# Kernel tuning notes

Measured on AMD Instinct MI355X. Metric: run time of the kernel, lower is better.

## Reference

```python
import jax, jax.numpy as jnp
import numpy as np
from jax.ops import segment_sum, segment_max

N_NODES = 50000
N_EDGES = 800000
B = 1024            # number of graphs
NODE_DIM = 21
ESM_DIM = 480
TAB_DIM = 7
H = 128             # hidden_dim
LSTM_H = H // 2     # 64 per direction
NEG_SLOPE = 0.2
BN_EPS = 1e-5


def setup_inputs() -> dict:
    key = jax.random.key(0)
    ks = iter(jax.random.split(key, 48))
    r = lambda shape, s=0.05: (s * jax.random.normal(next(ks), shape)).astype(jnp.float32)
    inp = {
        'x': jax.random.normal(next(ks), (N_NODES, NODE_DIM), dtype=jnp.float32),
        'edge_index': jax.random.randint(next(ks), (2, N_EDGES), 0, N_NODES, dtype=jnp.int64),
        'batch': jnp.sort(jax.random.randint(next(ks), (N_NODES,), 0, B, dtype=jnp.int64)),
        'esm_emb': jax.random.normal(next(ks), (B, ESM_DIM), dtype=jnp.float32),
        'tab_feats': jax.random.normal(next(ks), (B, TAB_DIM), dtype=jnp.float32),
        # GATConv 1 (heads=1)
        'gat1_W': r((H, NODE_DIM)), 'gat1_asrc': r((H,)), 'gat1_adst': r((H,)), 'gat1_b': r((H,)),
        # GATConv 2
        'gat2_W': r((H, H)), 'gat2_asrc': r((H,)), 'gat2_adst': r((H,)), 'gat2_b': r((H,)),
        # Bidirectional LSTM (seq_len=1, so a single cell step per direction)
        'lstm_Wih_f': r((4 * LSTM_H, ESM_DIM)), 'lstm_Whh_f': r((4 * LSTM_H, LSTM_H)),
        'lstm_bih_f': r((4 * LSTM_H,)), 'lstm_bhh_f': r((4 * LSTM_H,)),
        'lstm_Wih_r': r((4 * LSTM_H, ESM_DIM)), 'lstm_Whh_r': r((4 * LSTM_H, LSTM_H)),
        'lstm_bih_r': r((4 * LSTM_H,)), 'lstm_bhh_r': r((4 * LSTM_H,)),
        # tabular net
        'tab_W': r((64, TAB_DIM)), 'tab_b': r((64,)), 'tab_bn_g': jnp.ones((64,), jnp.float32), 'tab_bn_b': jnp.zeros((64,), jnp.float32),
        # fusion head
        'fus1_W': r((256, 320)), 'fus1_b': r((256,)), 'fus_bn_g': jnp.ones((256,), jnp.float32), 'fus_bn_b': jnp.zeros((256,), jnp.float32),
        'fus2_W': r((128, 256)), 'fus2_b': r((128,)),
        'fus3_W': r((1, 128)), 'fus3_b': r((1,)),
    }
    return inp


def _gat(h_in, src, dst, W, a_src, a_dst, bias):
    # PyG GATConv, heads=1, concat=True, self-loops already appended.
    h = h_in @ W.T                                  # [N, H]
    alpha_s = h @ a_src                             # [N]
    alpha_d = h @ a_dst                             # [N]
    e = jax.nn.leaky_relu(alpha_s[src] + alpha_d[dst], NEG_SLOPE)  # [E]
    m = segment_max(e, dst, num_segments=N_NODES)   # stable softmax per target
    ex = jnp.exp(e - m[dst])
    den = segment_sum(ex, dst, num_segments=N_NODES)
    coef = ex / (den[dst] + 1e-16)
    out = segment_sum(coef[:, None] * h[src], dst, num_segments=N_NODES)
    return out + bias


def _bn(x, g, b):
    # BatchNorm1d in training mode: biased batch statistics
    mu = jnp.mean(x, axis=0)
    var = jnp.var(x, axis=0)
    return (x - mu) * jax.lax.rsqrt(var + BN_EPS) * g + b


def _lstm_step(x, Wih, Whh, bih, bhh):
    # single step with zero initial (h, c); Whh term vanishes but kept for fidelity
    g = x @ Wih.T + bih + jnp.zeros((x.shape[0], Whh.shape[1]), x.dtype) @ Whh.T + bhh
    i, f, gg, o = jnp.split(g, 4, axis=1)           # PyTorch gate order i,f,g,o
    c = jax.nn.sigmoid(i) * jnp.tanh(gg)
    return jax.nn.sigmoid(o) * jnp.tanh(c)


def reference(x, edge_index, batch, esm_emb, tab_feats,
              gat1_W, gat1_asrc, gat1_adst, gat1_b,
              gat2_W, gat2_asrc, gat2_adst, gat2_b,
              lstm_Wih_f, lstm_Whh_f, lstm_bih_f, lstm_bhh_f,
              lstm_Wih_r, lstm_Whh_r, lstm_bih_r, lstm_bhh_r,
              tab_W, tab_b, tab_bn_g, tab_bn_b,
              fus1_W, fus1_b, fus_bn_g, fus_bn_b,
              fus2_W, fus2_b, fus3_W, fus3_b):
    sl = jnp.arange(N_NODES, dtype=edge_index.dtype)
    src = jnp.concatenate([edge_index[0], sl])      # add_self_loops=True default
    dst = jnp.concatenate([edge_index[1], sl])

    h1 = jax.nn.relu(_gat(x, src, dst, gat1_W, gat1_asrc, gat1_adst, gat1_b))
    h2 = jax.nn.relu(_gat(h1, src, dst, gat2_W, gat2_asrc, gat2_adst, gat2_b))

    counts = segment_sum(jnp.ones((N_NODES,), h2.dtype), batch, num_segments=B)
    graph_embed = segment_sum(h2, batch, num_segments=B) / jnp.maximum(counts, 1.0)[:, None]

    # bilstm over seq_len=1: output at last (only) step = concat(fwd, bwd)
    h_f = _lstm_step(esm_emb, lstm_Wih_f, lstm_Whh_f, lstm_bih_f, lstm_bhh_f)
    h_r = _lstm_step(esm_emb, lstm_Wih_r, lstm_Whh_r, lstm_bih_r, lstm_bhh_r)
    seq_embed = jnp.concatenate([h_f, h_r], axis=1)  # [B, 128]

    tab_embed = jax.nn.relu(_bn(tab_feats @ tab_W.T + tab_b, tab_bn_g, tab_bn_b))

    z = jnp.concatenate([graph_embed, seq_embed, tab_embed], axis=1)  # [B, 320]
    z = jax.nn.relu(_bn(z @ fus1_W.T + fus1_b, fus_bn_g, fus_bn_b))   # dropout: identity (eval)
    z = jax.nn.relu(z @ fus2_W.T + fus2_b)
    return z @ fus3_W.T + fus3_b                     # [B, 1]
```

## Files before the change

### kernel.cpp

```cpp
#include <hip/hip_runtime.h>
#include <hip/hip_bf16.h>

#define N_NODES 50000
#define N_PAD   50048
#define N_EDGES 800000
#define E_TOT   850000
#define NB      1024
#define ESM_DIM 480
#define HD      128
#define NBUCK   196
#define CAP     5120
#define EPB     3321
#define SC_BLK  256
#define CVT_BLK 256
#define BND_BLK 196
#define WC_BLK  16
#define TAB_BLK 4
#define G1B     782
#define LSTM_B  96
#define LG      384
#define AGG_GRID 12500
#define NL_BLK  512

typedef short short8 __attribute__((ext_vector_type(8)));
typedef unsigned short ushort8 __attribute__((ext_vector_type(8)));
typedef float f32x4 __attribute__((ext_vector_type(4)));

__device__ __forceinline__ float bf2f(unsigned int u) {
    union { unsigned int i; float f; } c; c.i = u << 16; return c.f;
}
__device__ __forceinline__ unsigned short f2bf(float f) {
    union { float f; unsigned int i; } c; c.f = f;
    unsigned int i = c.i;
    return (unsigned short)((i + 0x7FFFu + ((i >> 16) & 1u)) >> 16);
}
__device__ __forceinline__ void split2(float v, unsigned short& h, unsigned short& l) {
    h = f2bf(v);
    l = f2bf(v - bf2f(h));
}


__device__ void dev_scatter(const int* __restrict__ ei, int* __restrict__ gcur,
                            int* __restrict__ pairs, int blk) {
    __shared__ int hist[NBUCK];
    int t = threadIdx.x;
    for (int u = t; u < NBUCK; u += 256) hist[u] = 0;
    __syncthreads();
    int e0 = blk * EPB;
    int e1 = (e0 + EPB < E_TOT) ? e0 + EPB : E_TOT;
    for (int e = e0 + t; e < e1; e += 256) {
        int d = (e < N_EDGES) ? ei[N_EDGES + e] : (e - N_EDGES);
        atomicAdd(&hist[d >> 8], 1);
    }
    __syncthreads();
    for (int u = t; u < NBUCK; u += 256) {
        int c = hist[u];
        hist[u] = (c > 0) ? atomicAdd(&gcur[u], c) : 0;
    }
    __syncthreads();
    for (int e = e0 + t; e < e1; e += 256) {
        int s, d;
        if (e < N_EDGES) { s = ei[e]; d = ei[N_EDGES + e]; }
        else             { s = d = e - N_EDGES; }
        int bu = d >> 8;
        int pos = atomicAdd(&hist[bu], 1);
        pairs[bu * CAP + pos] = s | ((d & 255) << 16);
    }
}

__device__ void dev_cvt(const float* __restrict__ esm,
                        const float* __restrict__ Wf,
                        const float* __restrict__ Wr,
                        const float* __restrict__ W1,
                        unsigned short* __restrict__ esm_h, unsigned short* __restrict__ esm_l,
                        unsigned short* __restrict__ wg_h,  unsigned short* __restrict__ wg_l,
                        unsigned short* __restrict__ w1h,   unsigned short* __restrict__ w1l,
                        int blk) {
    int tid = blk * 256 + threadIdx.x;
    for (int u = tid; u < NB * 120; u += CVT_BLK * 256) {
        float4 v = ((const float4*)esm)[u];
        ushort4 h, l;
        split2(v.x, h.x, l.x); split2(v.y, h.y, l.y);
        split2(v.z, h.z, l.z); split2(v.w, h.w, l.w);
        ((ushort4*)esm_h)[u] = h; ((ushort4*)esm_l)[u] = l;
    }
    for (int u = tid; u < LG * 120; u += CVT_BLK * 256) {
        int n = u / 120, kk = u - n * 120;
        int rr = (n >= 192) ? n - 192 : n;
        const float* Ws = (n >= 192) ? Wr : Wf;
        int srow = (rr < 64) ? rr : rr + 64;
        float4 v = *(const float4*)&Ws[(size_t)srow * 480 + kk * 4];
        ushort4 h, l;
        split2(v.x, h.x, l.x); split2(v.y, h.y, l.y);
        split2(v.z, h.z, l.z); split2(v.w, h.w, l.w);
        ((ushort4*)wg_h)[u] = h; ((ushort4*)wg_l)[u] = l;
    }
    for (int u = tid; u < 128 * 32; u += CVT_BLK * 256) {
        int f = u >> 5, k = u & 31;
        float v = (k < 21) ? W1[f * 21 + k] : 0.f;
        unsigned short h, l;
        split2(v, h, l);
        w1h[u] = h; w1l[u] = l;
    }
}

__device__ void dev_tab4(const float* __restrict__ tf, const float* __restrict__ W,
                         const float* __restrict__ bias, const float* __restrict__ g,
                         const float* __restrict__ b, float* __restrict__ z, int blk) {
    __shared__ float ssum[16][16];
    __shared__ float ssq[16][16];
    int t = threadIdx.x;
    int rg = t >> 4, jl = t & 15;
    int j = blk * 16 + jl;
    float Wj[7];
#pragma unroll
    for (int k = 0; k < 7; ++k) Wj[k] = W[j * 7 + k];
    float bj = bias[j];
    float s = 0.f, q = 0.f;
    for (int rr = 0; rr < 64; ++rr) {
        int row = rg * 64 + rr;
        const float* xp = &tf[(size_t)row * 7];
        float a = bj;
#pragma unroll
        for (int k = 0; k < 7; ++k) a += xp[k] * Wj[k];
        s += a; q += a * a;
    }
    ssum[rg][jl] = s; ssq[rg][jl] = q;
    __syncthreads();
    for (int off = 8; off; off >>= 1) {
        if (rg < off) { ssum[rg][jl] += ssum[rg + off][jl]; ssq[rg][jl] += ssq[rg + off][jl]; }
        __syncthreads();
    }
    float mu = ssum[0][jl] * (1.f / 1024.f);
    float var = ssq[0][jl] * (1.f / 1024.f) - mu * mu;
    float sc = rsqrtf(var + 1e-5f) * g[j];
    float sh = b[j] - mu * sc;
    for (int rr = 0; rr < 64; ++rr) {
        int row = rg * 64 + rr;
        const float* xp = &tf[(size_t)row * 7];
        float a = bj;
#pragma unroll
        for (int k = 0; k < 7; ++k) a += xp[k] * Wj[k];
        z[(size_t)row * 320 + 256 + j] = fmaxf(a * sc + sh, 0.f);
    }
}

__global__ __launch_bounds__(256) void megaA(
        const int* __restrict__ ei, int* __restrict__ gcur, int* __restrict__ pairs,
        const float* __restrict__ esm, const float* __restrict__ Wih_f,
        const float* __restrict__ Wih_r, const float* __restrict__ gat1_W,
        unsigned short* __restrict__ esm_h, unsigned short* __restrict__ esm_l,
        unsigned short* __restrict__ wg_h,  unsigned short* __restrict__ wg_l,
        unsigned short* __restrict__ w1h,   unsigned short* __restrict__ w1l,
        const int* __restrict__ batch, int* __restrict__ gstart,
        const float* __restrict__ W2, unsigned short* __restrict__ Wb,
        const float* __restrict__ tf, const float* __restrict__ tab_W,
        const float* __restrict__ tab_b, const float* __restrict__ tab_g,
        const float* __restrict__ tab_bb, float* __restrict__ z) {
    int b = blockIdx.x, t = threadIdx.x;
    if (b < SC_BLK) {
        dev_scatter(ei, gcur, pairs, b);
    } else if (b < SC_BLK + CVT_BLK) {
        dev_cvt(esm, Wih_f, Wih_r, gat1_W, esm_h, esm_l, wg_h, wg_l, w1h, w1l, b - SC_BLK);
    } else if (b < SC_BLK + CVT_BLK + BND_BLK) {
        int i = (b - (SC_BLK + CVT_BLK)) * 256 + t;
        if (i >= N_NODES) return;
        int bb = batch[i];
        int bp = (i == 0) ? -1 : batch[i - 1];
        for (int g = bp + 1; g <= bb; ++g) gstart[g] = i;
        if (i == N_NODES - 1)
            for (int g = bb + 1; g <= NB; ++g) gstart[g] = N_NODES;
    } else if (b < SC_BLK + CVT_BLK + BND_BLK + WC_BLK) {
        int i = (b - (SC_BLK + CVT_BLK + BND_BLK)) * 256 + t;
        if (i >= 128 * 32) return;
        float4 v = ((const float4*)W2)[i];
        ((ushort4*)Wb)[i] = make_ushort4(f2bf(v.x), f2bf(v.y), f2bf(v.z), f2bf(v.w));
    } else {
        dev_tab4(tf, tab_W, tab_b, tab_g, tab_bb, z,
                 b - (SC_BLK + CVT_BLK + BND_BLK + WC_BLK));
    }
}


__device__ __forceinline__ float sigmoidf_(float x) { return 1.f / (1.f + __expf(-x)); }

__device__ void dev_gat1_mfma(const float* __restrict__ X,
                              const unsigned short* __restrict__ w1h,
                              const unsigned short* __restrict__ w1l,
                              const float* __restrict__ asrc, const float* __restrict__ adst,
                              unsigned short* __restrict__ out,
                              float* __restrict__ alpha_s, float* __restrict__ alpha_d,
                              int blk) {
    int t = threadIdx.x;
    int wid = t >> 6, L = t & 63, quad = L >> 4, lo = L & 15;
    int m0 = blk * 64 + wid * 16;
    int row = m0 + lo;
    const float* xr = X + (size_t)row * 21;
    int kbase = quad * 8;
    bool valid = row < N_NODES;
    float xv[8];
#pragma unroll
    for (int j = 0; j < 8; ++j) {
        int k = kbase + j;
        xv[j] = (valid && k < 21) ? xr[k] : 0.f;
    }
    short8 ah, al;
#pragma unroll
    for (int j = 0; j < 8; ++j) {
        unsigned short h, l;
        split2(xv[j], h, l);
        ah[j] = (short)h; al[j] = (short)l;
    }
    float as_p[4] = {0.f, 0.f, 0.f, 0.f};
    float ad_p[4] = {0.f, 0.f, 0.f, 0.f};
#pragma unroll
    for (int ft = 0; ft < 8; ++ft) {
        short8 bh = *(const short8*)&w1h[(ft * 16 + lo) * 32 + kbase];
        short8 bl = *(const short8*)&w1l[(ft * 16 + lo) * 32 + kbase];
        f32x4 acc = {0.f, 0.f, 0.f, 0.f};
        acc = __builtin_amdgcn_mfma_f32_16x16x32_bf16(ah, bh, acc, 0, 0, 0);
        acc = __builtin_amdgcn_mfma_f32_16x16x32_bf16(al, bh, acc, 0, 0, 0);
        acc = __builtin_amdgcn_mfma_f32_16x16x32_bf16(ah, bl, acc, 0, 0, 0);
        float asv = asrc[ft * 16 + lo];
        float adv = adst[ft * 16 + lo];
#pragma unroll
        for (int r = 0; r < 4; ++r) {
            int m = m0 + quad * 4 + r;
            out[(size_t)m * HD + ft * 16 + lo] = f2bf(acc[r]);
            as_p[r] += acc[r] * asv;
            ad_p[r] += acc[r] * adv;
        }
    }
#pragma unroll
    for (int off = 1; off < 16; off <<= 1) {
#pragma unroll
        for (int r = 0; r < 4; ++r) {
            as_p[r] += __shfl_xor(as_p[r], off);
            ad_p[r] += __shfl_xor(ad_p[r], off);
        }
    }
    if (lo == 0) {
#pragma unroll
        for (int r = 0; r < 4; ++r) {
            int m = m0 + quad * 4 + r;
            if (m < N_NODES) { alpha_s[m] = as_p[r]; alpha_d[m] = ad_p[r]; }
        }
    }
}

__device__ void dev_lstm_mfma(const unsigned short* __restrict__ Ah,
                              const unsigned short* __restrict__ Al,
                              const unsigned short* __restrict__ Bh,
                              const unsigned short* __restrict__ Bl,
                              float* __restrict__ G, int blk) {
    __shared__ unsigned short Bsh[64][104];
    __shared__ unsigned short Bsl[64][104];
    int t = threadIdx.x;
    int wid = t >> 6, L = t & 63, quad = L >> 4, lo = L & 15;
    int nt = blk % 6, mt = blk / 6;
    int m0 = mt * 64 + wid * 16;
    int n0 = nt * 64;
    f32x4 accs[4];
#pragma unroll
    for (int ft = 0; ft < 4; ++ft) accs[ft] = (f32x4){0.f, 0.f, 0.f, 0.f};
    const unsigned short* arh = Ah + (size_t)(m0 + lo) * ESM_DIM;
    const unsigned short* arl = Al + (size_t)(m0 + lo) * ESM_DIM;
    for (int c = 0; c < 5; ++c) {
        int k0c = c * 96;
        short8 ah[3], al[3];
#pragma unroll
        for (int ks = 0; ks < 3; ++ks) {
            ah[ks] = *(const short8*)&arh[k0c + ks * 32 + quad * 8];
            al[ks] = *(const short8*)&arl[k0c + ks * 32 + quad * 8];
        }
#pragma unroll
        for (int u = 0; u < 3; ++u) {
            int li = u * 2048 + t * 8;
            int row = li / 96, col = li % 96;
            *(ushort8*)&Bsh[row][col] =
                *(const ushort8*)&Bh[(size_t)(n0 + row) * ESM_DIM + k0c + col];
            *(ushort8*)&Bsl[row][col] =
                *(const ushort8*)&Bl[(size_t)(n0 + row) * ESM_DIM + k0c + col];
        }
        __syncthreads();
#pragma unroll
        for (int ks = 0; ks < 3; ++ks) {
#pragma unroll
            for (int ft = 0; ft < 4; ++ft) {
                short8 bh = *(const short8*)&Bsh[ft * 16 + lo][ks * 32 + quad * 8];
                short8 bl = *(const short8*)&Bsl[ft * 16 + lo][ks * 32 + quad * 8];
                accs[ft] = __builtin_amdgcn_mfma_f32_16x16x32_bf16(ah[ks], bh, accs[ft], 0, 0, 0);
                accs[ft] = __builtin_amdgcn_mfma_f32_16x16x32_bf16(al[ks], bh, accs[ft], 0, 0, 0);
                accs[ft] = __builtin_amdgcn_mfma_f32_16x16x32_bf16(ah[ks], bl, accs[ft], 0, 0, 0);
            }
        }
        __syncthreads();
    }
#pragma unroll
    for (int ft = 0; ft < 4; ++ft) {
#pragma unroll
        for (int r = 0; r < 4; ++r)
            G[(size_t)(m0 + quad * 4 + r) * LG + n0 + ft * 16 + lo] = accs[ft][r];
    }
}

__global__ __launch_bounds__(256) void megaB(
        const int* __restrict__ gcur, const int* __restrict__ pairs,
        int* __restrict__ row_beg, int* __restrict__ row_end, int* __restrict__ csr_src,
        const float* __restrict__ x,
        const unsigned short* __restrict__ w1h, const unsigned short* __restrict__ w1l,
        const float* __restrict__ gat1_as, const float* __restrict__ gat1_ad,
        unsigned short* __restrict__ h0, float* __restrict__ alpha_s, float* __restrict__ alpha_d,
        const unsigned short* __restrict__ esm_h, const unsigned short* __restrict__ esm_l,
        const unsigned short* __restrict__ wg_h,  const unsigned short* __restrict__ wg_l,
        float* __restrict__ g_lstm) {
    int b = blockIdx.x, t = threadIdx.x;
    if (b < NBUCK) {
        __shared__ int dc[256];
        __shared__ int wt[4];
        __shared__ int cur[256];
        int rs = b * CAP;
        int re = rs + gcur[b];
        dc[t] = 0;
        __syncthreads();
        for (int i = rs + t; i < re; i += 1024) {
            int i1 = i + 256, i2 = i + 512, i3 = i + 768;
            int p0 = pairs[i];
            int p1 = (i1 < re) ? pairs[i1] : 0;
            int p2 = (i2 < re) ? pairs[i2] : 0;
            int p3 = (i3 < re) ? pairs[i3] : 0;
            atomicAdd(&dc[p0 >> 16], 1);
            if (i1 < re) atomicAdd(&dc[p1 >> 16], 1);
            if (i2 < re) atomicAdd(&dc[p2 >> 16], 1);
            if (i3 < re) atomicAdd(&dc[p3 >> 16], 1);
        }
        __syncthreads();
        int v = dc[t];
        int lane = t & 63, wid = t >> 6;
        int sc = v;
#pragma unroll
        for (int off = 1; off < 64; off <<= 1) {
            int n = __shfl_up(sc, off);
            if (lane >= off) sc += n;
        }
        if (lane == 63) wt[wid] = sc;
        __syncthreads();
        int pref = 0;
        for (int ww = 0; ww < wid; ++ww) pref += wt[ww];
        int beg = rs + pref + sc - v;
        int node = b * 256 + t;
        if (node < N_NODES) { row_beg[node] = beg; row_end[node] = beg + v; }
        cur[t] = beg;
        __syncthreads();
        for (int i = rs + t; i < re; i += 1024) {
            int i1 = i + 256, i2 = i + 512, i3 = i + 768;
            int p0 = pairs[i];
            int p1 = (i1 < re) ? pairs[i1] : 0;
            int p2 = (i2 < re) ? pairs[i2] : 0;
            int p3 = (i3 < re) ? pairs[i3] : 0;
            int pos0 = atomicAdd(&cur[p0 >> 16], 1);
            csr_src[pos0] = p0 & 0xFFFF;
            if (i1 < re) { int pos = atomicAdd(&cur[p1 >> 16], 1); csr_src[pos] = p1 & 0xFFFF; }
            if (i2 < re) { int pos = atomicAdd(&cur[p2 >> 16], 1); csr_src[pos] = p2 & 0xFFFF; }
            if (i3 < re) { int pos = atomicAdd(&cur[p3 >> 16], 1); csr_src[pos] = p3 & 0xFFFF; }
        }
    } else if (b < NBUCK + LSTM_B) {
        dev_lstm_mfma(esm_h, esm_l, wg_h, wg_l, g_lstm, b - NBUCK);
    } else {
        dev_gat1_mfma(x, w1h, w1l, gat1_as, gat1_ad, h0, alpha_s, alpha_d,
                      b - (NBUCK + LSTM_B));
    }
}


__global__ __launch_bounds__(256) void gemm_mfma(const unsigned short* __restrict__ A,
                                                 const unsigned short* __restrict__ Wb,
                                                 const float* __restrict__ asrc,
                                                 const float* __restrict__ adst,
                                                 unsigned short* __restrict__ out,
                                                 float* __restrict__ alpha_s,
                                                 float* __restrict__ alpha_d, int M) {
    __shared__ unsigned short Wlds[128 * 136];
    int t = threadIdx.x;
    for (int u = t; u < 128 * 16; u += 256) {
        int row = u >> 4, seg = u & 15;
        *(ushort8*)&Wlds[row * 136 + seg * 8] = *(const ushort8*)&Wb[row * 128 + seg * 8];
    }
    __syncthreads();
    int wid = t >> 6, L = t & 63;
    int quad = L >> 4, lo = L & 15;
    int m0 = blockIdx.x * 64 + wid * 16;
    short8 afrag[4];
#pragma unroll
    for (int ch = 0; ch < 4; ++ch)
        afrag[ch] = *(const short8*)&A[(size_t)(m0 + lo) * HD + ch * 32 + quad * 8];
    float as_p[4] = {0.f, 0.f, 0.f, 0.f};
    float ad_p[4] = {0.f, 0.f, 0.f, 0.f};
#pragma unroll
    for (int ft = 0; ft < 8; ++ft) {
        f32x4 acc = {0.f, 0.f, 0.f, 0.f};
#pragma unroll
        for (int ch = 0; ch < 4; ++ch) {
            short8 b = *(const short8*)&Wlds[(ft * 16 + lo) * 136 + ch * 32 + quad * 8];
            acc = __builtin_amdgcn_mfma_f32_16x16x32_bf16(afrag[ch], b, acc, 0, 0, 0);
        }
        float asv = asrc[ft * 16 + lo];
        float adv = adst[ft * 16 + lo];
#pragma unroll
        for (int r = 0; r < 4; ++r) {
            int m = m0 + quad * 4 + r;
            if (m < M) out[(size_t)m * HD + ft * 16 + lo] = f2bf(acc[r]);
            as_p[r] += acc[r] * asv;
            ad_p[r] += acc[r] * adv;
        }
    }
#pragma unroll
    for (int off = 1; off < 16; off <<= 1) {
#pragma unroll
        for (int r = 0; r < 4; ++r) {
            as_p[r] += __shfl_xor(as_p[r], off);
            ad_p[r] += __shfl_xor(ad_p[r], off);
        }
    }
    if (lo == 0) {
#pragma unroll
        for (int r = 0; r < 4; ++r) {
            int m = m0 + quad * 4 + r;
            if (m < M) { alpha_s[m] = as_p[r]; alpha_d[m] = ad_p[r]; }
        }
    }
}


__global__ void gat_spmm(const unsigned short* __restrict__ h, const int* __restrict__ row_beg,
                         const int* __restrict__ row_end, const int* __restrict__ csr_src,
                         const float* __restrict__ alpha_s, const float* __restrict__ alpha_d,
                         const float* __restrict__ bias, unsigned short* __restrict__ outp,
                         const float* __restrict__ g_lstm,
                         const float* __restrict__ bihf, const float* __restrict__ bhhf,
                         const float* __restrict__ bihr, const float* __restrict__ bhhr,
                         float* __restrict__ z) {
    if (blockIdx.x >= AGG_GRID) {
        int idx = (blockIdx.x - AGG_GRID) * 256 + threadIdx.x;
        int bb = idx >> 7, jj = idx & 127;
        int dir = jj >> 6, j = jj & 63;
        const float* gb = g_lstm + (size_t)bb * LG + dir * 192;
        const float* bi = dir ? bihr : bihf;
        const float* bh = dir ? bhhr : bhhf;
        float gi = gb[j]        + bi[j]        + bh[j];
        float gg = gb[64 + j]   + bi[128 + j]  + bh[128 + j];
        float go = gb[128 + j]  + bi[192 + j]  + bh[192 + j];
        float c = sigmoidf_(gi) * tanhf(gg);
        z[(size_t)bb * 320 + 128 + jj] = sigmoidf_(go) * tanhf(c);
        return;
    }
    int w = (int)((blockIdx.x * (size_t)blockDim.x + threadIdx.x) >> 6);
    int lane = threadIdx.x & 63;
    if (w >= N_NODES) return;
    int grp = lane >> 4, l16 = lane & 15;
    int rs = row_beg[w], re = row_end[w];
    int deg = re - rs;
    float ad = alpha_d[w];
    float acc[8] = {0.f, 0.f, 0.f, 0.f, 0.f, 0.f, 0.f, 0.f};
    if (deg <= 64) {
        int s_reg = 0;
        float e = -1e30f;
        if (lane < deg) {
            s_reg = csr_src[rs + lane];
            float t0 = alpha_s[s_reg] + ad;
            e = (t0 > 0.f) ? t0 : 0.2f * t0;
        }
        float m = e;
#pragma unroll
        for (int off = 32; off; off >>= 1) m = fmaxf(m, __shfl_xor(m, off));
        float ex = (lane < deg) ? __expf(e - m) : 0.f;
        float den = ex;
#pragma unroll
        for (int off = 32; off; off >>= 1) den += __shfl_xor(den, off);
        float coef = ex / (den + 1e-16f);
        int i = rs + grp;
        for (; i + 4 < re; i += 8) {
            int idx = i - rs;
            float c0 = __shfl(coef, idx);
            int   s0 = __shfl(s_reg, idx);
            float c1 = __shfl(coef, idx + 4);
            int   s1 = __shfl(s_reg, idx + 4);
            ushort8 h0 = *(const ushort8*)&h[(size_t)s0 * HD + l16 * 8];
            ushort8 h1 = *(const ushort8*)&h[(size_t)s1 * HD + l16 * 8];
#pragma unroll
            for (int j = 0; j < 8; ++j) acc[j] += c0 * bf2f(h0[j]);
#pragma unroll
            for (int j = 0; j < 8; ++j) acc[j] += c1 * bf2f(h1[j]);
        }
        if (i < re) {
            int idx = i - rs;
            float c0 = __shfl(coef, idx);
            int   s0 = __shfl(s_reg, idx);
            ushort8 h0 = *(const ushort8*)&h[(size_t)s0 * HD + l16 * 8];
#pragma unroll
            for (int j = 0; j < 8; ++j) acc[j] += c0 * bf2f(h0[j]);
        }
    } else {
        float m = -1e30f;
        for (int i = rs + lane; i < re; i += 64) {
            int s = csr_src[i];
            float t0 = alpha_s[s] + ad;
            t0 = (t0 > 0.f) ? t0 : 0.2f * t0;
            m = fmaxf(m, t0);
        }
#pragma unroll
        for (int off = 32; off; off >>= 1) m = fmaxf(m, __shfl_xor(m, off));
        float den = 0.f;
        for (int i = rs + lane; i < re; i += 64) {
            int s = csr_src[i];
            float t0 = alpha_s[s] + ad;
            t0 = (t0 > 0.f) ? t0 : 0.2f * t0;
            den += __expf(t0 - m);
        }
#pragma unroll
        for (int off = 32; off; off >>= 1) den += __shfl_xor(den, off);
        float inv = 1.f / (den + 1e-16f);
        for (int i = rs + grp; i < re; i += 4) {
            int s = csr_src[i];
            float t0 = alpha_s[s] + ad;
            t0 = (t0 > 0.f) ? t0 : 0.2f * t0;
            float c = __expf(t0 - m) * inv;
            ushort8 hv = *(const ushort8*)&h[(size_t)s * HD + l16 * 8];
#pragma unroll
            for (int j = 0; j < 8; ++j) acc[j] += c * bf2f(hv[j]);
        }
    }
#pragma unroll
    for (int j = 0; j < 8; ++j) {
        acc[j] += __shfl_xor(acc[j], 16);
        acc[j] += __shfl_xor(acc[j], 32);
    }
    int f0 = l16 * 8 + grp * 2;
    float2 bv = *(const float2*)&bias[f0];
    float vx = fmaxf(acc[grp * 2]     + bv.x, 0.f);
    float vy = fmaxf(acc[grp * 2 + 1] + bv.y, 0.f);
    unsigned int pv = (unsigned int)f2bf(vx) | ((unsigned int)f2bf(vy) << 16);
    *(unsigned int*)&outp[(size_t)w * HD + f0] = pv;
}


__global__ void pool_kernel(const unsigned short* __restrict__ h, const int* __restrict__ start,
                            float* __restrict__ z) {
    int w = (int)((blockIdx.x * (size_t)blockDim.x + threadIdx.x) >> 6);
    int lane = threadIdx.x & 63;
    if (w >= NB) return;
    int grp = lane >> 4, l16 = lane & 15;
    int s0 = start[w], s1 = start[w + 1];
    float acc[8] = {0.f, 0.f, 0.f, 0.f, 0.f, 0.f, 0.f, 0.f};
    int n = s0 + grp;
    for (; n + 4 < s1; n += 8) {
        ushort8 a = *(const ushort8*)&h[(size_t)n * HD + l16 * 8];
        ushort8 b = *(const ushort8*)&h[(size_t)(n + 4) * HD + l16 * 8];
#pragma unroll
        for (int j = 0; j < 8; ++j) acc[j] += bf2f(a[j]);
#pragma unroll
        for (int j = 0; j < 8; ++j) acc[j] += bf2f(b[j]);
    }
    if (n < s1) {
        ushort8 a = *(const ushort8*)&h[(size_t)n * HD + l16 * 8];
#pragma unroll
        for (int j = 0; j < 8; ++j) acc[j] += bf2f(a[j]);
    }
#pragma unroll
    for (int j = 0; j < 8; ++j) {
        acc[j] += __shfl_xor(acc[j], 16);
        acc[j] += __shfl_xor(acc[j], 32);
    }
    float inv = 1.f / fmaxf((float)(s1 - s0), 1.f);
    int f0 = l16 * 8 + grp * 2;
    *(float2*)&z[(size_t)w * 320 + f0] =
        make_float2(acc[grp * 2] * inv, acc[grp * 2 + 1] * inv);
}
// ... 92 lines not shown
            *(float4*)&Ws[wf][wk] = *(const float4*)&W2[(size_t)wf * 256 + kc + wk];
        }
        __syncthreads();
#pragma unroll
        for (int k = 0; k < 32; ++k) {
            float w = Ws[f][k];
#pragma unroll
            for (int r = 0; r < 8; ++r) acc[r] += Xs[rh * 8 + r][k] * w;
        }
        __syncthreads();
    }
    float bv = b2[f], wv = W3[f];
    if (t < 16) rowsum[t] = 0.f;
    __syncthreads();
#pragma unroll
    for (int r = 0; r < 8; ++r) {
        float v = fmaxf(acc[r] + bv, 0.f) * wv;
#pragma unroll
        for (int off = 32; off; off >>= 1) v += __shfl_xor(v, off);
        if ((t & 63) == 0) atomicAdd(&rowsum[rh * 8 + r], v);
    }
    __syncthreads();
    if (t < 16) out[r0 + t] = rowsum[t] + b3[0];
}


extern "C" void kernel_launch(void* const* d_in, const int* in_sizes, int n_in,
                              void* d_out, int out_size, void* d_ws, size_t ws_size,
                              hipStream_t stream) {
    const float* x        = (const float*)d_in[0];
    const int*   ei       = (const int*)d_in[1];
    const int*   batch    = (const int*)d_in[2];
    const float* esm      = (const float*)d_in[3];
    const float* tabf     = (const float*)d_in[4];
    const float* gat1_W   = (const float*)d_in[5];
    const float* gat1_as  = (const float*)d_in[6];
    const float* gat1_ad  = (const float*)d_in[7];
    const float* gat1_b   = (const float*)d_in[8];
    const float* gat2_W   = (const float*)d_in[9];
    const float* gat2_as  = (const float*)d_in[10];
    const float* gat2_ad  = (const float*)d_in[11];
    const float* gat2_b   = (const float*)d_in[12];
    const float* Wih_f    = (const float*)d_in[13];
    const float* bih_f    = (const float*)d_in[15];
    const float* bhh_f    = (const float*)d_in[16];
    const float* Wih_r    = (const float*)d_in[17];
    const float* bih_r    = (const float*)d_in[19];
    const float* bhh_r    = (const float*)d_in[20];
    const float* tab_W    = (const float*)d_in[21];
    const float* tab_b    = (const float*)d_in[22];
    const float* tab_g    = (const float*)d_in[23];
    const float* tab_bb   = (const float*)d_in[24];
    const float* fus1_W   = (const float*)d_in[25];
    const float* fus_g    = (const float*)d_in[27];
    const float* fus_bb   = (const float*)d_in[28];
    const float* fus2_W   = (const float*)d_in[29];
    const float* fus2_b   = (const float*)d_in[30];
    const float* fus3_W   = (const float*)d_in[31];
    const float* fus3_b   = (const float*)d_in[32];
    float* out = (float*)d_out;

    char* ws = (char*)d_ws;
    size_t off = 0;
    auto alloc = [&](size_t bytes) -> char* {
        char* p = ws + off;
        off += (bytes + 255) & ~(size_t)255;
        return p;
    };
    unsigned short* h0_bf = (unsigned short*)alloc((size_t)N_PAD * HD * 2);
    unsigned short* hA_bf = (unsigned short*)alloc((size_t)N_PAD * HD * 2);
    unsigned short* h2_bf = (unsigned short*)alloc((size_t)N_PAD * HD * 2);
    unsigned short* h_act = (unsigned short*)alloc((size_t)N_NODES * HD * 2);
    float* alpha_s = (float*)alloc((size_t)N_NODES * 4);
    float* alpha_d = (float*)alloc((size_t)N_NODES * 4);
    unsigned short* w2bf = (unsigned short*)alloc((size_t)HD * HD * 2);
    int*   row_beg = (int*)alloc((size_t)N_NODES * 4);
    int*   row_end = (int*)alloc((size_t)N_NODES * 4);
    int*   csr_src = (int*)alloc((size_t)NBUCK * CAP * 4);
    int*   pairs   = (int*)alloc((size_t)NBUCK * CAP * 4);
    int*   gstart  = (int*)alloc((size_t)(NB + 1) * 4);
    float* z1pre   = (float*)alloc((size_t)NB * 256 * 4);
    float* z       = (float*)alloc((size_t)NB * 320 * 4);
    float* g_lstm  = (float*)alloc((size_t)NB * LG * 4);
    unsigned short* esm_h = (unsigned short*)alloc((size_t)NB * ESM_DIM * 2);
    unsigned short* esm_l = (unsigned short*)alloc((size_t)NB * ESM_DIM * 2);
    unsigned short* wg_h  = (unsigned short*)alloc((size_t)LG * ESM_DIM * 2);
    unsigned short* wg_l  = (unsigned short*)alloc((size_t)LG * ESM_DIM * 2);
    unsigned short* w1h   = (unsigned short*)alloc((size_t)128 * 32 * 2);
    unsigned short* w1l   = (unsigned short*)alloc((size_t)128 * 32 * 2);
    int*   gcur    = (int*)alloc((size_t)NBUCK * 4);
    float* colsum  = (float*)alloc((size_t)256 * 4);
    float* colsq   = (float*)alloc((size_t)256 * 4);
    size_t zero_len = (size_t)((char*)colsq + 256 * 4 - (char*)gcur);
    hipMemsetAsync(gcur, 0, zero_len, stream);

    megaA<<<SC_BLK + CVT_BLK + BND_BLK + WC_BLK + TAB_BLK, 256, 0, stream>>>(
        ei, gcur, pairs, esm, Wih_f, Wih_r, gat1_W,
        esm_h, esm_l, wg_h, wg_l, w1h, w1l,
        batch, gstart, gat2_W, w2bf,
        tabf, tab_W, tab_b, tab_g, tab_bb, z);

    megaB<<<NBUCK + LSTM_B + G1B, 256, 0, stream>>>(
        gcur, pairs, row_beg, row_end, csr_src,
        x, w1h, w1l, gat1_as, gat1_ad, h0_bf, alpha_s, alpha_d,
        esm_h, esm_l, wg_h, wg_l, g_lstm);

    gat_spmm<<<AGG_GRID + NL_BLK, 256, 0, stream>>>(h0_bf, row_beg, row_end, csr_src,
                                                    alpha_s, alpha_d, gat1_b, hA_bf,
                                                    g_lstm, bih_f, bhh_f, bih_r, bhh_r, z);

    gemm_mfma<<<N_PAD / 64, 256, 0, stream>>>(hA_bf, w2bf, gat2_as, gat2_ad,
                                              h2_bf, alpha_s, alpha_d, N_NODES);

    gat_spmm<<<AGG_GRID, 256, 0, stream>>>(h2_bf, row_beg, row_end, csr_src,
                                           alpha_s, alpha_d, gat2_b, h_act,
                                           g_lstm, bih_f, bhh_f, bih_r, bhh_r, z);

    pool_kernel<<<(NB + 3) / 4, 256, 0, stream>>>(h_act, gstart, z);

    fus1_stats<<<dim3(64, 4), 256, 0, stream>>>(z, fus1_W, z1pre, colsum, colsq);

    fus2_final<<<64, 256, 0, stream>>>(z1pre, colsum, colsq, fus_g, fus_bb,
                                       fus2_W, fus2_b, fus3_W, fus3_b, out);

    (void)in_sizes; (void)n_in; (void)out_size; (void)ws_size;
}
```

Measured before the change: 292.3 us.

## Fuse bf16 split conversion into GAT1/LSTM consumers and move them into first launch

Removes the separate conversion pass that pre-split esm embeddings and weights into bf16 hi/lo buffers. The GAT1 and LSTM MFMA kernels now read fp32 and split in-register, and both move into the first mega-launch, so the second launch only builds the CSR. The edge scatter caches each thread's packed edges in registers to avoid re-reading edge_index, and the SpMM inner loop is unrolled to four neighbours. The cost is redundant conversion work per block and higher register pressure in the scatter and SpMM.

```diff
diff --git a/kernel.cpp b/kernel.cpp
--- a/kernel.cpp
+++ b/kernel.cpp
@@ -12,7 +12,6 @@
 #define CAP     5120
 #define EPB     3321
 #define SC_BLK  256
-#define CVT_BLK 256
 #define BND_BLK 196
 #define WC_BLK  16
 #define TAB_BLK 4
@@ -48,9 +47,18 @@
     __syncthreads();
     int e0 = blk * EPB;
     int e1 = (e0 + EPB < E_TOT) ? e0 + EPB : E_TOT;
-    for (int e = e0 + t; e < e1; e += 256) {
-        int d = (e < N_EDGES) ? ei[N_EDGES + e] : (e - N_EDGES);
-        atomicAdd(&hist[d >> 8], 1);
+    int ec[13];
+#pragma unroll
+    for (int u = 0; u < 13; ++u) {
+        int e = e0 + t + u * 256;
+        if (e < e1) {
+            int s, d;
+            if (e < N_EDGES) { s = ei[e]; d = ei[N_EDGES + e]; }
+            else             { s = d = e - N_EDGES; }
+            int bu = d >> 8;
+            ec[u] = s | ((d & 255) << 16) | (bu << 24);
+            atomicAdd(&hist[bu], 1);
+        }
     }
     __syncthreads();
     for (int u = t; u < NBUCK; u += 256) {
@@ -58,135 +66,20 @@
         hist[u] = (c > 0) ? atomicAdd(&gcur[u], c) : 0;
     }
     __syncthreads();
-    for (int e = e0 + t; e < e1; e += 256) {
-        int s, d;
-        if (e < N_EDGES) { s = ei[e]; d = ei[N_EDGES + e]; }
-        else             { s = d = e - N_EDGES; }
-        int bu = d >> 8;
-        int pos = atomicAdd(&hist[bu], 1);
-        pairs[bu * CAP + pos] = s | ((d & 255) << 16);
-    }
-}
-
-__device__ void dev_cvt(const float* __restrict__ esm,
-                        const float* __restrict__ Wf,
-                        const float* __restrict__ Wr,
-                        const float* __restrict__ W1,
-                        unsigned short* __restrict__ esm_h, unsigned short* __restrict__ esm_l,
-                        unsigned short* __restrict__ wg_h,  unsigned short* __restrict__ wg_l,
-                        unsigned short* __restrict__ w1h,   unsigned short* __restrict__ w1l,
-                        int blk) {
-    int tid = blk * 256 + threadIdx.x;
-    for (int u = tid; u < NB * 120; u += CVT_BLK * 256) {
-        float4 v = ((const float4*)esm)[u];
-        ushort4 h, l;
-        split2(v.x, h.x, l.x); split2(v.y, h.y, l.y);
-        split2(v.z, h.z, l.z); split2(v.w, h.w, l.w);
-        ((ushort4*)esm_h)[u] = h; ((ushort4*)esm_l)[u] = l;
-    }
-    for (int u = tid; u < LG * 120; u += CVT_BLK * 256) {
-        int n = u / 120, kk = u - n * 120;
-        int rr = (n >= 192) ? n - 192 : n;
-        const float* Ws = (n >= 192) ? Wr : Wf;
-        int srow = (rr < 64) ? rr : rr + 64;
-        float4 v = *(const float4*)&Ws[(size_t)srow * 480 + kk * 4];
-        ushort4 h, l;
-        split2(v.x, h.x, l.x); split2(v.y, h.y, l.y);
-        split2(v.z, h.z, l.z); split2(v.w, h.w, l.w);
-        ((ushort4*)wg_h)[u] = h; ((ushort4*)wg_l)[u] = l;
-    }
-    for (int u = tid; u < 128 * 32; u += CVT_BLK * 256) {
-        int f = u >> 5, k = u & 31;
-        float v = (k < 21) ? W1[f * 21 + k] : 0.f;
-        unsigned short h, l;
-        split2(v, h, l);
-        w1h[u] = h; w1l[u] = l;
-    }
-}
-
-__device__ void dev_tab4(const float* __restrict__ tf, const float* __restrict__ W,
-                         const float* __restrict__ bias, const float* __restrict__ g,
-                         const float* __restrict__ b, float* __restrict__ z, int blk) {
-    __shared__ float ssum[16][16];
-    __shared__ float ssq[16][16];
-    int t = threadIdx.x;
-    int rg = t >> 4, jl = t & 15;
-    int j = blk * 16 + jl;
-    float Wj[7];
-#pragma unroll
-    for (int k = 0; k < 7; ++k) Wj[k] = W[j * 7 + k];
-    float bj = bias[j];
-    float s = 0.f, q = 0.f;
-    for (int rr = 0; rr < 64; ++rr) {
-        int row = rg * 64 + rr;
-        const float* xp = &tf[(size_t)row * 7];
-        float a = bj;
-#pragma unroll
-        for (int k = 0; k < 7; ++k) a += xp[k] * Wj[k];
-        s += a; q += a * a;
-    }
-    ssum[rg][jl] = s; ssq[rg][jl] = q;
-    __syncthreads();
-    for (int off = 8; off; off >>= 1) {
-        if (rg < off) { ssum[rg][jl] += ssum[rg + off][jl]; ssq[rg][jl] += ssq[rg + off][jl]; }
-        __syncthreads();
-    }
-    float mu = ssum[0][jl] * (1.f / 1024.f);
-    float var = ssq[0][jl] * (1.f / 1024.f) - mu * mu;
-    float sc = rsqrtf(var + 1e-5f) * g[j];
-    float sh = b[j] - mu * sc;
-    for (int rr = 0; rr < 64; ++rr) {
-        int row = rg * 64 + rr;
-        const float* xp = &tf[(size_t)row * 7];
-        float a = bj;
-#pragma unroll
-        for (int k = 0; k < 7; ++k) a += xp[k] * Wj[k];
-        z[(size_t)row * 320 + 256 + j] = fmaxf(a * sc + sh, 0.f);
-    }
-}
-
-__global__ __launch_bounds__(256) void megaA(
-        const int* __restrict__ ei, int* __restrict__ gcur, int* __restrict__ pairs,
-        const float* __restrict__ esm, const float* __restrict__ Wih_f,
-        const float* __restrict__ Wih_r, const float* __restrict__ gat1_W,
-        unsigned short* __restrict__ esm_h, unsigned short* __restrict__ esm_l,
-        unsigned short* __restrict__ wg_h,  unsigned short* __restrict__ wg_l,
-        unsigned short* __restrict__ w1h,   unsigned short* __restrict__ w1l,
-        const int* __restrict__ batch, int* __restrict__ gstart,
-        const float* __restrict__ W2, unsigned short* __restrict__ Wb,
-        const float* __restrict__ tf, const float* __restrict__ tab_W,
-        const float* __restrict__ tab_b, const float* __restrict__ tab_g,
-        const float* __restrict__ tab_bb, float* __restrict__ z) {
-    int b = blockIdx.x, t = threadIdx.x;
-    if (b < SC_BLK) {
-        dev_scatter(ei, gcur, pairs, b);
-    } else if (b < SC_BLK + CVT_BLK) {
-        dev_cvt(esm, Wih_f, Wih_r, gat1_W, esm_h, esm_l, wg_h, wg_l, w1h, w1l, b - SC_BLK);
-    } else if (b < SC_BLK + CVT_BLK + BND_BLK) {
-        int i = (b - (SC_BLK + CVT_BLK)) * 256 + t;
-        if (i >= N_NODES) return;
-        int bb = batch[i];
-        int bp = (i == 0) ? -1 : batch[i - 1];
-        for (int g = bp + 1; g <= bb; ++g) gstart[g] = i;
-        if (i == N_NODES - 1)
-            for (int g = bb + 1; g <= NB; ++g) gstart[g] = N_NODES;
-    } else if (b < SC_BLK + CVT_BLK + BND_BLK + WC_BLK) {
-        int i = (b - (SC_BLK + CVT_BLK + BND_BLK)) * 256 + t;
-        if (i >= 128 * 32) return;
-        float4 v = ((const float4*)W2)[i];
-        ((ushort4*)Wb)[i] = make_ushort4(f2bf(v.x), f2bf(v.y), f2bf(v.z), f2bf(v.w));
-    } else {
-        dev_tab4(tf, tab_W, tab_b, tab_g, tab_bb, z,
-                 b - (SC_BLK + CVT_BLK + BND_BLK + WC_BLK));
-    }
-}
-
-
-__device__ __forceinline__ float sigmoidf_(float x) { return 1.f / (1.f + __expf(-x)); }
+#pragma unroll
+    for (int u = 0; u < 13; ++u) {
+        int e = e0 + t + u * 256;
+        if (e < e1) {
+            int val = ec[u];
+            int bu = ((unsigned)val) >> 24;
+            int pos = atomicAdd(&hist[bu], 1);
+            pairs[bu * CAP + pos] = val & 0xFFFFFF;
+        }
+    }
+}
 
 __device__ void dev_gat1_mfma(const float* __restrict__ X,
-                              const unsigned short* __restrict__ w1h,
-                              const unsigned short* __restrict__ w1l,
+                              const float* __restrict__ W1,
                               const float* __restrict__ asrc, const float* __restrict__ adst,
                               unsigned short* __restrict__ out,
                               float* __restrict__ alpha_s, float* __restrict__ alpha_d,
@@ -198,25 +91,29 @@
     const float* xr = X + (size_t)row * 21;
     int kbase = quad * 8;
     bool valid = row < N_NODES;
-    float xv[8];
+    short8 ah, al;
 #pragma unroll
     for (int j = 0; j < 8; ++j) {
         int k = kbase + j;
-        xv[j] = (valid && k < 21) ? xr[k] : 0.f;
-    }
-    short8 ah, al;
-#pragma unroll
-    for (int j = 0; j < 8; ++j) {
+        float v = (valid && k < 21) ? xr[k] : 0.f;
         unsigned short h, l;
-        split2(xv[j], h, l);
+        split2(v, h, l);
         ah[j] = (short)h; al[j] = (short)l;
     }
     float as_p[4] = {0.f, 0.f, 0.f, 0.f};
     float ad_p[4] = {0.f, 0.f, 0.f, 0.f};
 #pragma unroll
     for (int ft = 0; ft < 8; ++ft) {
-        short8 bh = *(const short8*)&w1h[(ft * 16 + lo) * 32 + kbase];
-        short8 bl = *(const short8*)&w1l[(ft * 16 + lo) * 32 + kbase];
+        const float* wr = W1 + (ft * 16 + lo) * 21;
+        short8 bh, bl;
+#pragma unroll
+        for (int j = 0; j < 8; ++j) {
+            int k = kbase + j;
+            float v = (k < 21) ? wr[k] : 0.f;
+            unsigned short h, l;
+            split2(v, h, l);
+            bh[j] = (short)h; bl[j] = (short)l;
+        }
         f32x4 acc = {0.f, 0.f, 0.f, 0.f};
         acc = __builtin_amdgcn_mfma_f32_16x16x32_bf16(ah, bh, acc, 0, 0, 0);
         acc = __builtin_amdgcn_mfma_f32_16x16x32_bf16(al, bh, acc, 0, 0, 0);
@@ -248,10 +145,9 @@
     }
 }
 
-__device__ void dev_lstm_mfma(const unsigned short* __restrict__ Ah,
-                              const unsigned short* __restrict__ Al,
-                              const unsigned short* __restrict__ Bh,
-                              const unsigned short* __restrict__ Bl,
+__device__ void dev_lstm_mfma(const float* __restrict__ esm,
+                              const float* __restrict__ Wf,
+                              const float* __restrict__ Wr,
                               float* __restrict__ G, int blk) {
     __shared__ unsigned short Bsh[64][104];
     __shared__ unsigned short Bsl[64][104];
@@ -263,24 +159,37 @@
     f32x4 accs[4];
 #pragma unroll
     for (int ft = 0; ft < 4; ++ft) accs[ft] = (f32x4){0.f, 0.f, 0.f, 0.f};
-    const unsigned short* arh = Ah + (size_t)(m0 + lo) * ESM_DIM;
-    const unsigned short* arl = Al + (size_t)(m0 + lo) * ESM_DIM;
+    const float* ar = esm + (size_t)(m0 + lo) * ESM_DIM;
     for (int c = 0; c < 5; ++c) {
         int k0c = c * 96;
         short8 ah[3], al[3];
 #pragma unroll
         for (int ks = 0; ks < 3; ++ks) {
-            ah[ks] = *(const short8*)&arh[k0c + ks * 32 + quad * 8];
-            al[ks] = *(const short8*)&arl[k0c + ks * 32 + quad * 8];
-        }
-#pragma unroll
-        for (int u = 0; u < 3; ++u) {
-            int li = u * 2048 + t * 8;
-            int row = li / 96, col = li % 96;
-            *(ushort8*)&Bsh[row][col] =
-                *(const ushort8*)&Bh[(size_t)(n0 + row) * ESM_DIM + k0c + col];
-            *(ushort8*)&Bsl[row][col] =
-                *(const ushort8*)&Bl[(size_t)(n0 + row) * ESM_DIM + k0c + col];
+            const float* ap = &ar[k0c + ks * 32 + quad * 8];
+            float4 v0 = *(const float4*)ap;
+            float4 v1 = *(const float4*)(ap + 4);
+            float av[8] = {v0.x, v0.y, v0.z, v0.w, v1.x, v1.y, v1.z, v1.w};
+#pragma unroll
+            for (int j = 0; j < 8; ++j) {
+                unsigned short h, l;
+                split2(av[j], h, l);
+                ah[ks][j] = (short)h; al[ks][j] = (short)l;
+            }
+        }
+#pragma unroll
+        for (int u = 0; u < 6; ++u) {
+            int li = u * 256 + t;
+            int rowb = li / 24, colb = (li % 24) * 4;
+            int n = n0 + rowb;
+            int rr = (n >= 192) ? n - 192 : n;
+            const float* Wsrc = (n >= 192) ? Wr : Wf;
+            int srow = (rr < 64) ? rr : rr + 64;
+            float4 v = *(const float4*)&Wsrc[(size_t)srow * ESM_DIM + k0c + colb];
+            ushort4 h, l;
+            split2(v.x, h.x, l.x); split2(v.y, h.y, l.y);
+            split2(v.z, h.z, l.z); split2(v.w, h.w, l.w);
+            *(ushort4*)&Bsh[rowb][colb] = h;
+            *(ushort4*)&Bsl[rowb][colb] = l;
         }
         __syncthreads();
 #pragma unroll
@@ -304,71 +213,139 @@
     }
 }
 
+__device__ void dev_tab4(const float* __restrict__ tf, const float* __restrict__ W,
+                         const float* __restrict__ bias, const float* __restrict__ g,
+                         const float* __restrict__ b, float* __restrict__ z, int blk) {
+    __shared__ float ssum[16][16];
+    __shared__ float ssq[16][16];
+    int t = threadIdx.x;
+    int rg = t >> 4, jl = t & 15;
+    int j = blk * 16 + jl;
+    float Wj[7];
+#pragma unroll
+    for (int k = 0; k < 7; ++k) Wj[k] = W[j * 7 + k];
+    float bj = bias[j];
+    float s = 0.f, q = 0.f;
+    for (int rr = 0; rr < 64; ++rr) {
+        int row = rg * 64 + rr;
+        const float* xp = &tf[(size_t)row * 7];
+        float a = bj;
+#pragma unroll
+        for (int k = 0; k < 7; ++k) a += xp[k] * Wj[k];
+        s += a; q += a * a;
+    }
+    ssum[rg][jl] = s; ssq[rg][jl] = q;
+    __syncthreads();
+    for (int off = 8; off; off >>= 1) {
+        if (rg < off) { ssum[rg][jl] += ssum[rg + off][jl]; ssq[rg][jl] += ssq[rg + off][jl]; }
+        __syncthreads();
+    }
+    float mu = ssum[0][jl] * (1.f / 1024.f);
+    float var = ssq[0][jl] * (1.f / 1024.f) - mu * mu;
+    float sc = rsqrtf(var + 1e-5f) * g[j];
+    float sh = b[j] - mu * sc;
+    for (int rr = 0; rr < 64; ++rr) {
+        int row = rg * 64 + rr;
+        const float* xp = &tf[(size_t)row * 7];
+        float a = bj;
+#pragma unroll
+        for (int k = 0; k < 7; ++k) a += xp[k] * Wj[k];
+        z[(size_t)row * 320 + 256 + j] = fmaxf(a * sc + sh, 0.f);
+    }
+}
+
+__global__ __launch_bounds__(256) void megaA(
+        const int* __restrict__ ei, int* __restrict__ gcur, int* __restrict__ pairs,
+        const float* __restrict__ x, const float* __restrict__ gat1_W,
+        const float* __restrict__ gat1_as, const float* __restrict__ gat1_ad,
+        unsigned short* __restrict__ h0, float* __restrict__ alpha_s, float* __restrict__ alpha_d,
+        const float* __restrict__ esm, const float* __restrict__ Wih_f,
+        const float* __restrict__ Wih_r, float* __restrict__ g_lstm,
+        const int* __restrict__ batch, int* __restrict__ gstart,
+        const float* __restrict__ W2, unsigned short* __restrict__ Wb,
+        const float* __restrict__ tf, const float* __restrict__ tab_W,
+        const float* __restrict__ tab_b, const float* __restrict__ tab_g,
+        const float* __restrict__ tab_bb, float* __restrict__ z) {
+    int b = blockIdx.x, t = threadIdx.x;
+    if (b < SC_BLK) {
+        dev_scatter(ei, gcur, pairs, b);
+    } else if (b < SC_BLK + G1B) {
+        dev_gat1_mfma(x, gat1_W, gat1_as, gat1_ad, h0, alpha_s, alpha_d, b - SC_BLK);
+    } else if (b < SC_BLK + G1B + LSTM_B) {
+        dev_lstm_mfma(esm, Wih_f, Wih_r, g_lstm, b - (SC_BLK + G1B));
+    } else if (b < SC_BLK + G1B + LSTM_B + BND_BLK) {
+        int i = (b - (SC_BLK + G1B + LSTM_B)) * 256 + t;
+        if (i >= N_NODES) return;
+        int bb = batch[i];
+        int bp = (i == 0) ? -1 : batch[i - 1];
+        for (int g = bp + 1; g <= bb; ++g) gstart[g] = i;
+        if (i == N_NODES - 1)
+            for (int g = bb + 1; g <= NB; ++g) gstart[g] = N_NODES;
+    } else if (b < SC_BLK + G1B + LSTM_B + BND_BLK + WC_BLK) {
+        int i = (b - (SC_BLK + G1B + LSTM_B + BND_BLK)) * 256 + t;
+        if (i >= 128 * 32) return;
+        float4 v = ((const float4*)W2)[i];
+        ((ushort4*)Wb)[i] = make_ushort4(f2bf(v.x), f2bf(v.y), f2bf(v.z), f2bf(v.w));
+    } else {
+        dev_tab4(tf, tab_W, tab_b, tab_g, tab_bb, z,
+                 b - (SC_BLK + G1B + LSTM_B + BND_BLK + WC_BLK));
+    }
+}
+
+
+__device__ __forceinline__ float sigmoidf_(float x) { return 1.f / (1.f + __expf(-x)); }
+
 __global__ __launch_bounds__(256) void megaB(
         const int* __restrict__ gcur, const int* __restrict__ pairs,
-        int* __restrict__ row_beg, int* __restrict__ row_end, int* __restrict__ csr_src,
-        const float* __restrict__ x,
-        const unsigned short* __restrict__ w1h, const unsigned short* __restrict__ w1l,
-        const float* __restrict__ gat1_as, const float* __restrict__ gat1_ad,
-        unsigned short* __restrict__ h0, float* __restrict__ alpha_s, float* __restrict__ alpha_d,
-        const unsigned short* __restrict__ esm_h, const unsigned short* __restrict__ esm_l,
-        const unsigned short* __restrict__ wg_h,  const unsigned short* __restrict__ wg_l,
-        float* __restrict__ g_lstm) {
+        int* __restrict__ row_beg, int* __restrict__ row_end, int* __restrict__ csr_src) {
     int b = blockIdx.x, t = threadIdx.x;
-    if (b < NBUCK) {
-        __shared__ int dc[256];
-        __shared__ int wt[4];
-        __shared__ int cur[256];
-        int rs = b * CAP;
-        int re = rs + gcur[b];
-        dc[t] = 0;
-        __syncthreads();
-        for (int i = rs + t; i < re; i += 1024) {
-            int i1 = i + 256, i2 = i + 512, i3 = i + 768;
-            int p0 = pairs[i];
-            int p1 = (i1 < re) ? pairs[i1] : 0;
-            int p2 = (i2 < re) ? pairs[i2] : 0;
-            int p3 = (i3 < re) ? pairs[i3] : 0;
-            atomicAdd(&dc[p0 >> 16], 1);
-            if (i1 < re) atomicAdd(&dc[p1 >> 16], 1);
-            if (i2 < re) atomicAdd(&dc[p2 >> 16], 1);
-            if (i3 < re) atomicAdd(&dc[p3 >> 16], 1);
-        }
-        __syncthreads();
-        int v = dc[t];
-        int lane = t & 63, wid = t >> 6;
-        int sc = v;
-#pragma unroll
-        for (int off = 1; off < 64; off <<= 1) {
-            int n = __shfl_up(sc, off);
-            if (lane >= off) sc += n;
-        }
-        if (lane == 63) wt[wid] = sc;
-        __syncthreads();
-        int pref = 0;
-        for (int ww = 0; ww < wid; ++ww) pref += wt[ww];
-        int beg = rs + pref + sc - v;
-        int node = b * 256 + t;
-        if (node < N_NODES) { row_beg[node] = beg; row_end[node] = beg + v; }
-        cur[t] = beg;
-        __syncthreads();
-        for (int i = rs + t; i < re; i += 1024) {
-            int i1 = i + 256, i2 = i + 512, i3 = i + 768;
-            int p0 = pairs[i];
-            int p1 = (i1 < re) ? pairs[i1] : 0;
-            int p2 = (i2 < re) ? pairs[i2] : 0;
-            int p3 = (i3 < re) ? pairs[i3] : 0;
-            int pos0 = atomicAdd(&cur[p0 >> 16], 1);
-            csr_src[pos0] = p0 & 0xFFFF;
-            if (i1 < re) { int pos = atomicAdd(&cur[p1 >> 16], 1); csr_src[pos] = p1 & 0xFFFF; }
-            if (i2 < re) { int pos = atomicAdd(&cur[p2 >> 16], 1); csr_src[pos] = p2 & 0xFFFF; }
-            if (i3 < re) { int pos = atomicAdd(&cur[p3 >> 16], 1); csr_src[pos] = p3 & 0xFFFF; }
-        }
-    } else if (b < NBUCK + LSTM_B) {
-        dev_lstm_mfma(esm_h, esm_l, wg_h, wg_l, g_lstm, b - NBUCK);
-    } else {
-        dev_gat1_mfma(x, w1h, w1l, gat1_as, gat1_ad, h0, alpha_s, alpha_d,
-                      b - (NBUCK + LSTM_B));
+    __shared__ int dc[256];
+    __shared__ int wt[4];
+    __shared__ int cur[256];
+    int rs = b * CAP;
+    int re = rs + gcur[b];
+    dc[t] = 0;
+    __syncthreads();
+    for (int i = rs + t; i < re; i += 1024) {
+        int i1 = i + 256, i2 = i + 512, i3 = i + 768;
+        int p0 = pairs[i];
+        int p1 = (i1 < re) ? pairs[i1] : 0;
+        int p2 = (i2 < re) ? pairs[i2] : 0;
+        int p3 = (i3 < re) ? pairs[i3] : 0;
+        atomicAdd(&dc[p0 >> 16], 1);
+        if (i1 < re) atomicAdd(&dc[p1 >> 16], 1);
+        if (i2 < re) atomicAdd(&dc[p2 >> 16], 1);
+        if (i3 < re) atomicAdd(&dc[p3 >> 16], 1);
+    }
+    __syncthreads();
+    int v = dc[t];
+    int lane = t & 63, wid = t >> 6;
+    int sc = v;
+#pragma unroll
+    for (int off = 1; off < 64; off <<= 1) {
+        int n = __shfl_up(sc, off);
+        if (lane >= off) sc += n;
+    }
+    if (lane == 63) wt[wid] = sc;
+    __syncthreads();
+    int pref = 0;
+    for (int ww = 0; ww < wid; ++ww) pref += wt[ww];
+    int beg = rs + pref + sc - v;
+    int node = b * 256 + t;
+    if (node < N_NODES) { row_beg[node] = beg; row_end[node] = beg + v; }
+    cur[t] = beg;
+    __syncthreads();
+    for (int i = rs + t; i < re; i += 1024) {
+        int i1 = i + 256, i2 = i + 512, i3 = i + 768;
+        int p0 = pairs[i];
+        int p1 = (i1 < re) ? pairs[i1] : 0;
+        int p2 = (i2 < re) ? pairs[i2] : 0;
+        int p3 = (i3 < re) ? pairs[i3] : 0;
+        int pos0 = atomicAdd(&cur[p0 >> 16], 1);
+        csr_src[pos0] = p0 & 0xFFFF;
+        if (i1 < re) { int pos = atomicAdd(&cur[p1 >> 16], 1); csr_src[pos] = p1 & 0xFFFF; }
+        if (i2 < re) { int pos = atomicAdd(&cur[p2 >> 16], 1); csr_src[pos] = p2 & 0xFFFF; }
+        if (i3 < re) { int pos = atomicAdd(&cur[p3 >> 16], 1); csr_src[pos] = p3 & 0xFFFF; }
     }
 }
 
@@ -479,20 +456,26 @@
         for (int off = 32; off; off >>= 1) den += __shfl_xor(den, off);
         float coef = ex / (den + 1e-16f);
         int i = rs + grp;
-        for (; i + 4 < re; i += 8) {
+        for (; i + 12 < re; i += 16) {
             int idx = i - rs;
-            float c0 = __shfl(coef, idx);
-            int   s0 = __shfl(s_reg, idx);
-            float c1 = __shfl(coef, idx + 4);
-            int   s1 = __shfl(s_reg, idx + 4);
+            float c0 = __shfl(coef, idx);       int s0 = __shfl(s_reg, idx);
+            float c1 = __shfl(coef, idx + 4);   int s1 = __shfl(s_reg, idx + 4);
+            float c2 = __shfl(coef, idx + 8);   int s2 = __shfl(s_reg, idx + 8);
+            float c3 = __shfl(coef, idx + 12);  int s3 = __shfl(s_reg, idx + 12);
             ushort8 h0 = *(const ushort8*)&h[(size_t)s0 * HD + l16 * 8];
             ushort8 h1 = *(const ushort8*)&h[(size_t)s1 * HD + l16 * 8];
+            ushort8 h2 = *(const ushort8*)&h[(size_t)s2 * HD + l16 * 8];
+            ushort8 h3 = *(const ushort8*)&h[(size_t)s3 * HD + l16 * 8];
 #pragma unroll
             for (int j = 0; j < 8; ++j) acc[j] += c0 * bf2f(h0[j]);
 #pragma unroll
             for (int j = 0; j < 8; ++j) acc[j] += c1 * bf2f(h1[j]);
-        }
-        if (i < re) {
+#pragma unroll
+            for (int j = 0; j < 8; ++j) acc[j] += c2 * bf2f(h2[j]);
+#pragma unroll
+            for (int j = 0; j < 8; ++j) acc[j] += c3 * bf2f(h3[j]);
+        }
+        for (; i < re; i += 4) {
             int idx = i - rs;
             float c0 = __shfl(coef, idx);
             int   s0 = __shfl(s_reg, idx);
@@ -751,28 +734,18 @@
     float* z1pre   = (float*)alloc((size_t)NB * 256 * 4);
     float* z       = (float*)alloc((size_t)NB * 320 * 4);
     float* g_lstm  = (float*)alloc((size_t)NB * LG * 4);
-    unsigned short* esm_h = (unsigned short*)alloc((size_t)NB * ESM_DIM * 2);
-    unsigned short* esm_l = (unsigned short*)alloc((size_t)NB * ESM_DIM * 2);
-    unsigned short* wg_h  = (unsigned short*)alloc((size_t)LG * ESM_DIM * 2);
-    unsigned short* wg_l  = (unsigned short*)alloc((size_t)LG * ESM_DIM * 2);
-    unsigned short* w1h   = (unsigned short*)alloc((size_t)128 * 32 * 2);
-    unsigned short* w1l   = (unsigned short*)alloc((size_t)128 * 32 * 2);
     int*   gcur    = (int*)alloc((size_t)NBUCK * 4);
     float* colsum  = (float*)alloc((size_t)256 * 4);
     float* colsq   = (float*)alloc((size_t)256 * 4);
     size_t zero_len = (size_t)((char*)colsq + 256 * 4 - (char*)gcur);
     hipMemsetAsync(gcur, 0, zero_len, stream);
 
-    megaA<<<SC_BLK + CVT_BLK + BND_BLK + WC_BLK + TAB_BLK, 256, 0, stream>>>(
-        ei, gcur, pairs, esm, Wih_f, Wih_r, gat1_W,
-        esm_h, esm_l, wg_h, wg_l, w1h, w1l,
-        batch, gstart, gat2_W, w2bf,
+    megaA<<<SC_BLK + G1B + LSTM_B + BND_BLK + WC_BLK + TAB_BLK, 256, 0, stream>>>(
+        ei, gcur, pairs, x, gat1_W, gat1_as, gat1_ad, h0_bf, alpha_s, alpha_d,
+        esm, Wih_f, Wih_r, g_lstm, batch, gstart, gat2_W, w2bf,
         tabf, tab_W, tab_b, tab_g, tab_bb, z);
 
-    megaB<<<NBUCK + LSTM_B + G1B, 256, 0, stream>>>(
-        gcur, pairs, row_beg, row_end, csr_src,
-        x, w1h, w1l, gat1_as, gat1_ad, h0_bf, alpha_s, alpha_d,
-        esm_h, esm_l, wg_h, wg_l, g_lstm);
+    megaB<<<NBUCK, 256, 0, stream>>>(gcur, pairs, row_beg, row_end, csr_src);
 
     gat_spmm<<<AGG_GRID + NL_BLK, 256, 0, stream>>>(h0_bf, row_beg, row_end, csr_src,
                                                     alpha_s, alpha_d, gat1_b, hA_bf,
```

New measurement: 306.5 us. 1.05x slower.
